# Performance work log

Hardware: AMD Instinct MI355X
Metric: run time of the kernel (lower is better)

## Reference

```python
import jax, jax.numpy as jnp
import numpy as np

BN_EPS = 1e-5
NN_CHUNK = 1024  # unknown points processed per distance-matrix tile


def _batch_ids(cnt, total):
    # contiguous per-batch layout -> batch id of each point via cumsum/searchsorted
    return jnp.searchsorted(jnp.cumsum(cnt), jnp.arange(total), side='right')


def three_nn(unknown, known, ub_id, kb_id):
    """Ragged brute-force 3-NN. Returns (squared dists [N,3], global idx [N,3])."""
    N = unknown.shape[0]
    nchunk = N // NN_CHUNK
    u = unknown.reshape(nchunk, NN_CHUNK, 3)
    ub = ub_id.reshape(nchunk, NN_CHUNK)

    def body(args):
        uc, bc = args
        d2 = jnp.sum((uc[:, None, :] - known[None, :, :]) ** 2, axis=-1)  # [chunk, M]
        d2 = jnp.where(bc[:, None] == kb_id[None, :], d2, jnp.inf)  # mask cross-batch pairs
        neg_d, idx = jax.lax.top_k(-d2, 3)
        return -neg_d, idx

    d2, idx = jax.lax.map(body, (u, ub))
    return d2.reshape(N, 3), idx.reshape(N, 3)


def three_interpolate(known_feats, idx, weight):
    # gather [N,3,C] then inverse-distance weighted sum -> [N,C]
    gathered = known_feats[idx]  # [N,3,C]
    return jnp.einsum('nkc,nk->nc', gathered, weight)


def conv_bn_relu(x, W, gamma, beta):
    # 1x1 Conv2d over [1,C,N,1] == pointwise matmul; BN (training stats) over points
    h = x @ W.T  # [N, C_out]
    mean = jnp.mean(h, axis=0)
    var = jnp.mean((h - mean) ** 2, axis=0)  # biased, as torch BN normalization
    h = (h - mean) * jax.lax.rsqrt(var + BN_EPS) * gamma + beta
    return jax.nn.relu(h)


def setup_inputs() -> dict:
    key = jax.random.key(0)
    ks = jax.random.split(key, 10)
    B, Nper, Mper, C1, C2 = 4, 16384, 4096, 128, 256
    N, M = B * Nper, B * Mper
    unknown = jax.random.normal(ks[0], (N, 3), jnp.float32) * 10.0
    known = jax.random.normal(ks[1], (M, 3), jnp.float32) * 10.0
    unknown_feats = jax.random.normal(ks[2], (N, C1), jnp.float32)
    known_feats = jax.random.normal(ks[3], (M, C2), jnp.float32)
    unknown_batch_cnt = jnp.full((B,), Nper, jnp.int32)
    known_batch_cnt = jnp.full((B,), Mper, jnp.int32)
    Cin = C1 + C2  # 384
    W1 = jax.random.normal(ks[4], (256, Cin), jnp.float32) * (1.0 / np.sqrt(Cin))
    W2 = jax.random.normal(ks[5], (256, 256), jnp.float32) * (1.0 / np.sqrt(256))
    g1 = jnp.ones((256,), jnp.float32); b1 = jnp.zeros((256,), jnp.float32)
    g2 = jnp.ones((256,), jnp.float32); b2 = jnp.zeros((256,), jnp.float32)
    return {"unknown": unknown, "unknown_batch_cnt": unknown_batch_cnt,
            "known": known, "known_batch_cnt": known_batch_cnt,
            "unknown_feats": unknown_feats, "known_feats": known_feats,
            "W1": W1, "g1": g1, "b1": b1, "W2": W2, "g2": g2, "b2": b2}


def reference(unknown, unknown_batch_cnt, known, known_batch_cnt,
              unknown_feats, known_feats, W1, g1, b1, W2, g2, b2):
    ub_id = _batch_ids(unknown_batch_cnt, unknown.shape[0])
    kb_id = _batch_ids(known_batch_cnt, known.shape[0])
    dist, idx = three_nn(unknown, known, ub_id, kb_id)  # squared dists, as CUDA kernel
    dist_recip = 1.0 / (dist + 1e-8)
    weight = dist_recip / jnp.sum(dist_recip, axis=-1, keepdims=True)
    interpolated = three_interpolate(known_feats, idx, weight)  # [N, C2]
    new_features = jnp.concatenate([interpolated, unknown_feats], axis=1)  # [N, C2+C1]
    new_features = conv_bn_relu(new_features, W1, g1, b1)
    new_features = conv_bn_relu(new_features, W2, g2, b2)
    return new_features  # [N, 256]
```

## Files before the change

### kernel.cpp

```cpp
#include <hip/hip_runtime.h>
#include <math.h>

typedef __attribute__((ext_vector_type(8))) short short8;
typedef __attribute__((ext_vector_type(4))) float f32x4;

#define INF 3.0e38f

__device__ __forceinline__ unsigned short f2bf(float x) {
    union { float f; unsigned u; } v; v.f = x;
    unsigned r = v.u + 0x7FFF + ((v.u >> 16) & 1);
    return (unsigned short)(r >> 16);
}

__device__ __forceinline__ float dist2(float ux, float uy, float uz, float4 k) {
    float dx = ux - k.x, dy = uy - k.y, dz = uz - k.z;
    return __builtin_fmaf(dx, dx, __builtin_fmaf(dy, dy, dz * dz));
}

__global__ __launch_bounds__(256) void knn3_kernel(
    const float* __restrict__ unk, const float* __restrict__ kn,
    const int* __restrict__ ucnt, const int* __restrict__ kcnt,
    int B, int N, float* __restrict__ wgt, int* __restrict__ idxo)
{
    __shared__ float4 kxyz[1024];
    __shared__ float md[4][64][3];
    __shared__ float d2g[64];
    __shared__ unsigned long long mk[4][64][3];

    int tid = threadIdx.x;
    int s = tid >> 6;
    int lane = tid & 63;
    int pbase = blockIdx.x * 64;
    int p = pbase + lane;

    int cum = 0, bb = 0;
    for (int i = 0; i < B; i++) { int c = ucnt[i]; if (pbase >= cum) bb = i; cum += c; }
    int kstart = 0;
    for (int i = 0; i < bb; i++) kstart += kcnt[i];
    int kend = kstart + kcnt[bb];

    float ux = unk[p * 3 + 0], uy = unk[p * 3 + 1], uz = unk[p * 3 + 2];

    float d0 = INF, d1 = INF, d2 = INF;
    auto upd = [&](float e) {
        float m0 = fmaxf(e, d0);
        float m1 = fmaxf(e, d1);
        d0 = fminf(e, d0);
        d1 = fminf(m0, d1);
        d2 = fminf(m1, d2);
    };

    for (int t0g = kstart; t0g < kend; t0g += 1024) {
        int cnt = min(1024, kend - t0g);
        __syncthreads();
        for (int f = tid; f < cnt * 3; f += 256) {
            int pt = f / 3, c = f - pt * 3;
            ((float*)&kxyz[pt])[c] = kn[(size_t)(t0g + pt) * 3 + c];
        }
        __syncthreads();

        int qlen = cnt >> 2;
        int base = s * qlen;
        for (int i = 0; i < qlen; i += 4) {
            float e0 = dist2(ux, uy, uz, kxyz[base + i]);
            float e1 = dist2(ux, uy, uz, kxyz[base + i + 1]);
            float e2 = dist2(ux, uy, uz, kxyz[base + i + 2]);
            float e3 = dist2(ux, uy, uz, kxyz[base + i + 3]);
            upd(e0); upd(e1); upd(e2); upd(e3);
        }
    }

    md[s][lane][0] = d0; md[s][lane][1] = d1; md[s][lane][2] = d2;
    __syncthreads();
    if (tid < 64) {
        float v0 = INF, v1 = INF, v2 = INF;
#pragma unroll
        for (int w = 0; w < 4; w++)
#pragma unroll
            for (int k = 0; k < 3; k++) {
                float e = md[w][tid][k];
                float m0 = fmaxf(e, v0);
                float m1 = fmaxf(e, v1);
                v0 = fminf(e, v0);
                v1 = fminf(m0, v1);
                v2 = fminf(m1, v2);
            }
        d2g[tid] = v2;
    }
    __syncthreads();
    float thr = d2g[lane];

    unsigned long long s0 = ~0ULL, s1 = ~0ULL, s2 = ~0ULL;
    auto insK = [&](unsigned long long k) {
        bool c0 = k < s0;
        unsigned long long t0 = c0 ? k : s0;
        unsigned long long t1 = c0 ? s0 : k;
        bool c1 = t1 < s1;
        unsigned long long u0 = c1 ? t1 : s1;
        unsigned long long u1 = c1 ? s1 : t1;
        s0 = t0; s1 = u0;
        s2 = u1 < s2 ? u1 : s2;
    };
    auto mkkey = [](float e, int gj) {
        return ((unsigned long long)__float_as_uint(e) << 32) | (unsigned)gj;
    };

    for (int t0g = kstart; t0g < kend; t0g += 1024) {
        int cnt = min(1024, kend - t0g);
        __syncthreads();
        for (int f = tid; f < cnt * 3; f += 256) {
            int pt = f / 3, c = f - pt * 3;
            ((float*)&kxyz[pt])[c] = kn[(size_t)(t0g + pt) * 3 + c];
        }
        __syncthreads();

        int qlen = cnt >> 2;
        int base = s * qlen;
        for (int i = 0; i < qlen; i += 4) {
            float e0 = dist2(ux, uy, uz, kxyz[base + i]);
            float e1 = dist2(ux, uy, uz, kxyz[base + i + 1]);
            float e2 = dist2(ux, uy, uz, kxyz[base + i + 2]);
            float e3 = dist2(ux, uy, uz, kxyz[base + i + 3]);
            float m4 = fminf(fminf(e0, e1), fminf(e2, e3));
            if (m4 <= thr) {
                int gj = t0g + base + i;
                insK(mkkey(e0, gj + 0));
                insK(mkkey(e1, gj + 1));
                insK(mkkey(e2, gj + 2));
                insK(mkkey(e3, gj + 3));
            }
        }
    }

    mk[s][lane][0] = s0; mk[s][lane][1] = s1; mk[s][lane][2] = s2;
    __syncthreads();

    if (tid < 64) {
        s0 = s1 = s2 = ~0ULL;
#pragma unroll
        for (int qq = 0; qq < 4; qq++)
#pragma unroll
            for (int kk = 0; kk < 3; kk++)
                insK(mk[qq][tid][kk]);

        float dd0 = __uint_as_float((unsigned)(s0 >> 32));
        float dd1 = __uint_as_float((unsigned)(s1 >> 32));
        float dd2 = __uint_as_float((unsigned)(s2 >> 32));
        float r0 = 1.0f / (dd0 + 1e-8f);
        float r1 = 1.0f / (dd1 + 1e-8f);
        float r2 = 1.0f / (dd2 + 1e-8f);
        float rs = 1.0f / (r0 + r1 + r2);
        int pp = pbase + tid;
        wgt[pp * 3 + 0] = r0 * rs;
        wgt[pp * 3 + 1] = r1 * rs;
        wgt[pp * 3 + 2] = r2 * rs;
        idxo[pp * 3 + 0] = (int)(unsigned)s0;
        idxo[pp * 3 + 1] = (int)(unsigned)s1;
        idxo[pp * 3 + 2] = (int)(unsigned)s2;
    }
}

__global__ __launch_bounds__(256) void build_a1_kernel(
    const float* __restrict__ wgt, const int* __restrict__ idxv,
    const float* __restrict__ kfeat, const float* __restrict__ ufeat,
    unsigned short* __restrict__ A1, int N)
{
    int t = blockIdx.x * 256 + threadIdx.x;
    int p = t >> 6, c4 = t & 63;
    if (p >= N) return;
    float w0 = wgt[p * 3 + 0], w1 = wgt[p * 3 + 1], w2 = wgt[p * 3 + 2];
    int j0 = idxv[p * 3 + 0], j1 = idxv[p * 3 + 1], j2 = idxv[p * 3 + 2];
    float4 v0 = ((const float4*)(kfeat + (size_t)j0 * 256))[c4];
    float4 v1 = ((const float4*)(kfeat + (size_t)j1 * 256))[c4];
    float4 v2 = ((const float4*)(kfeat + (size_t)j2 * 256))[c4];
    ushort4 ob;
    ob.x = f2bf(v0.x * w0 + v1.x * w1 + v2.x * w2);
    ob.y = f2bf(v0.y * w0 + v1.y * w1 + v2.y * w2);
    ob.z = f2bf(v0.z * w0 + v1.z * w1 + v2.z * w2);
    ob.w = f2bf(v0.w * w0 + v1.w * w1 + v2.w * w2);
    *(ushort4*)(A1 + (size_t)p * 384 + c4 * 4) = ob;
    float2 u = ((const float2*)(ufeat + (size_t)p * 128))[c4];
    ushort2 ub; ub.x = f2bf(u.x); ub.y = f2bf(u.y);
    *(ushort2*)(A1 + (size_t)p * 384 + 256 + c4 * 2) = ub;
}

__global__ __launch_bounds__(256) void wconv_kernel(
    const float* __restrict__ W1, const float* __restrict__ W2,
    unsigned short* __restrict__ W1b, unsigned short* __restrict__ W2b,
    int n1, int n2)
{
    int i = blockIdx.x * 256 + threadIdx.x;
    if (i < n1) W1b[i] = f2bf(W1[i]);
    int j = i - n1;
    if (j >= 0 && j < n2) W2b[j] = f2bf(W2[j]);
}

template <int K, int MODE>
__global__ __launch_bounds__(256) void gemm_bf16_kernel(
    const void* __restrict__ Av, const unsigned short* __restrict__ W,
    const float* __restrict__ scale, const float* __restrict__ shift,
    float* __restrict__ C, float* __restrict__ gsum, float* __restrict__ gsq)
{
    __shared__ unsigned short As[128 * 40];
    __shared__ unsigned short Bs[128 * 40];
    __shared__ float colsum[128];
    __shared__ float colsq[128];

    int tid = threadIdx.x;
    int w = tid >> 6, lane = tid & 63;
    int r = w >> 1, cq = w & 1;
    int m16 = lane & 15, q = lane >> 4;
    int bm = blockIdx.x * 128, bn = blockIdx.y * 128;

    f32x4 acc[4][4];
#pragma unroll
    for (int i = 0; i < 4; i++)
#pragma unroll
        for (int j = 0; j < 4; j++) acc[i][j] = (f32x4){0.f, 0.f, 0.f, 0.f};

#pragma unroll
    for (int k0 = 0; k0 < K; k0 += 32) {
        __syncthreads();
#pragma unroll
        for (int i = 0; i < 2; i++) {
            int id = tid + i * 256;
            int row = id >> 2, kc = (id & 3) * 8;
            if (MODE == 0) {
                *(short8*)&As[row * 40 + kc] =
                    *(const short8*)((const unsigned short*)Av +
                                     (size_t)(bm + row) * K + k0 + kc);
            } else {
                const float* Af = (const float*)Av;
                float4 v0 = *(const float4*)(Af + (size_t)(bm + row) * K + k0 + kc);
                float4 v1 = *(const float4*)(Af + (size_t)(bm + row) * K + k0 + kc + 4);
                float4 s0 = *(const float4*)(scale + k0 + kc);
                float4 s1 = *(const float4*)(scale + k0 + kc + 4);
                float4 t0 = *(const float4*)(shift + k0 + kc);
                float4 t1 = *(const float4*)(shift + k0 + kc + 4);
                ushort4 o0, o1;
                o0.x = f2bf(fmaxf(v0.x * s0.x + t0.x, 0.f));
                o0.y = f2bf(fmaxf(v0.y * s0.y + t0.y, 0.f));
                o0.z = f2bf(fmaxf(v0.z * s0.z + t0.z, 0.f));
                o0.w = f2bf(fmaxf(v0.w * s0.w + t0.w, 0.f));
                o1.x = f2bf(fmaxf(v1.x * s1.x + t1.x, 0.f));
                o1.y = f2bf(fmaxf(v1.y * s1.y + t1.y, 0.f));
                o1.z = f2bf(fmaxf(v1.z * s1.z + t1.z, 0.f));
                o1.w = f2bf(fmaxf(v1.w * s1.w + t1.w, 0.f));
                *(ushort4*)&As[row * 40 + kc] = o0;
                *(ushort4*)&As[row * 40 + kc + 4] = o1;
            }
            *(short8*)&Bs[row * 40 + kc] =
                *(const short8*)(W + (size_t)(bn + row) * K + k0 + kc);
        }
        __syncthreads();

        short8 af[4], bf[4];
#pragma unroll
        for (int sub = 0; sub < 4; sub++) {
            af[sub] = *(const short8*)&As[(r * 64 + sub * 16 + m16) * 40 + q * 8];
            bf[sub] = *(const short8*)&Bs[(cq * 64 + sub * 16 + m16) * 40 + q * 8];
        }
#pragma unroll
        for (int sm = 0; sm < 4; sm++)
#pragma unroll
            for (int sn = 0; sn < 4; sn++)
                acc[sm][sn] = __builtin_amdgcn_mfma_f32_16x16x32_bf16(
                    af[sm], bf[sn], acc[sm][sn], 0, 0, 0);
    }

    int row0 = bm + r * 64 + q * 4;
    int col0 = bn + cq * 64 + m16;
#pragma unroll
    for (int sm = 0; sm < 4; sm++)
#pragma unroll
        for (int sn = 0; sn < 4; sn++) {
            f32x4 v = acc[sm][sn];
#pragma unroll
            for (int reg = 0; reg < 4; reg++)
                C[(size_t)(row0 + sm * 16 + reg) * 256 + col0 + sn * 16] = v[reg];
        }

    __syncthreads();
    if (tid < 128) { colsum[tid] = 0.f; colsq[tid] = 0.f; }
    __syncthreads();
#pragma unroll
    for (int sn = 0; sn < 4; sn++) {
        float sacc = 0.f, qacc = 0.f;
#pragma unroll
        for (int sm = 0; sm < 4; sm++) {
            f32x4 v = acc[sm][sn];
#pragma unroll
            for (int reg = 0; reg < 4; reg++) {
                sacc += v[reg];
                qacc += v[reg] * v[reg];
            }
        }
        int lc = cq * 64 + sn * 16 + m16;
        atomicAdd(&colsum[lc], sacc);
        atomicAdd(&colsq[lc], qacc);
    }
    __syncthreads();
    if (tid < 128) {
        atomicAdd(&gsum[bn + tid], colsum[tid]);
        atomicAdd(&gsq[bn + tid], colsq[tid]);
    }
}

__global__ void bn_finalize_kernel(
    const float* __restrict__ sum, const float* __restrict__ sumsq,
    const float* __restrict__ g, const float* __restrict__ bta, float invN,
    float* __restrict__ scale, float* __restrict__ shift)
{
    int c = threadIdx.x;
    float mean = sum[c] * invN;
    float var = sumsq[c] * invN - mean * mean;
    float sc = g[c] * rsqrtf(var + 1e-5f);
    scale[c] = sc;
    shift[c] = bta[c] - mean * sc;
}

__global__ __launch_bounds__(256) void final_act_kernel(
    const float* __restrict__ h2, const float* __restrict__ scale,
    const float* __restrict__ shift, float* __restrict__ out, int total4)
{
    int i = blockIdx.x * 256 + threadIdx.x;
    if (i >= total4) return;
    int c4 = i & 63;
    float4 v = ((const float4*)h2)[i];
    float4 s = ((const float4*)scale)[c4];
    float4 t = ((const float4*)shift)[c4];
    float4 o;
    o.x = fmaxf(v.x * s.x + t.x, 0.0f);
    o.y = fmaxf(v.y * s.y + t.y, 0.0f);
    o.z = fmaxf(v.z * s.z + t.z, 0.0f);
    o.w = fmaxf(v.w * s.w + t.w, 0.0f);
    ((float4*)out)[i] = o;
}

extern "C" void kernel_launch(void* const* d_in, const int* in_sizes, int n_in,
                              void* d_out, int out_size, void* d_ws, size_t ws_size,
                              hipStream_t stream)
{
    const float* unknown = (const float*)d_in[0];
    const int*   ucnt    = (const int*)d_in[1];
    const float* known   = (const float*)d_in[2];
    const int*   kcnt    = (const int*)d_in[3];
    const float* ufeat   = (const float*)d_in[4];
    const float* kfeat   = (const float*)d_in[5];
    const float* W1      = (const float*)d_in[6];
    const float* g1      = (const float*)d_in[7];
    const float* b1      = (const float*)d_in[8];
    const float* W2      = (const float*)d_in[9];
    const float* g2      = (const float*)d_in[10];
    const float* b2      = (const float*)d_in[11];

    int N = in_sizes[0] / 3;
    int B = in_sizes[1];

    char* ws = (char*)d_ws;
    size_t off = 0;
    float* wgt = (float*)(ws + off);            off += (size_t)N * 3 * 4;
    int*   idxb = (int*)(ws + off);             off += (size_t)N * 3 * 4;
    float* stats = (float*)(ws + off);          off += 8 * 256 * 4;
    float* sum1 = stats,         *sq1 = stats + 256;
    float* scale1 = stats + 512, *shift1 = stats + 768;
    float* sum2 = stats + 1024,  *sq2 = stats + 1280;
    float* scale2 = stats + 1536, *shift2 = stats + 1792;
    unsigned short* W1b = (unsigned short*)(ws + off);  off += 256 * 384 * 2;
    unsigned short* W2b = (unsigned short*)(ws + off);  off += 256 * 256 * 2;
    off = (off + 255) & ~(size_t)255;
    unsigned short* A1 = (unsigned short*)(ws + off);
    float* h2 = (float*)(ws + off);
    float* h1 = (float*)d_out;

    hipMemsetAsync(stats, 0, 8 * 256 * 4, stream);

    knn3_kernel<<<N / 64, 256, 0, stream>>>(unknown, known, ucnt, kcnt,
                                            B, N, wgt, idxb);
    wconv_kernel<<<(256 * 384 + 256 * 256 + 255) / 256, 256, 0, stream>>>(
        W1, W2, W1b, W2b, 256 * 384, 256 * 256);
    build_a1_kernel<<<N / 4, 256, 0, stream>>>(wgt, idxb, kfeat, ufeat, A1, N);
    gemm_bf16_kernel<384, 0><<<dim3(N / 128, 2), 256, 0, stream>>>(
        A1, W1b, nullptr, nullptr, h1, sum1, sq1);
    bn_finalize_kernel<<<1, 256, 0, stream>>>(sum1, sq1, g1, b1, 1.0f / N,
                                              scale1, shift1);
    gemm_bf16_kernel<256, 1><<<dim3(N / 128, 2), 256, 0, stream>>>(
        h1, W2b, scale1, shift1, h2, sum2, sq2);
    bn_finalize_kernel<<<1, 256, 0, stream>>>(sum2, sq2, g2, b2, 1.0f / N,
                                              scale2, shift2);
    final_act_kernel<<<N / 4, 256, 0, stream>>>(h2, scale2, shift2,
                                                (float*)d_out, N * 64);
}
```

Before: 413.6 us.

## Read known points via wave-uniform scalar loads instead of LDS staging in kNN

```diff
diff --git a/kernel.cpp b/kernel.cpp
--- a/kernel.cpp
+++ b/kernel.cpp
@@ -12,23 +12,17 @@
     return (unsigned short)(r >> 16);
 }
 
-__device__ __forceinline__ float dist2(float ux, float uy, float uz, float4 k) {
-    float dx = ux - k.x, dy = uy - k.y, dz = uz - k.z;
-    return __builtin_fmaf(dx, dx, __builtin_fmaf(dy, dy, dz * dz));
-}
-
 __global__ __launch_bounds__(256) void knn3_kernel(
     const float* __restrict__ unk, const float* __restrict__ kn,
     const int* __restrict__ ucnt, const int* __restrict__ kcnt,
     int B, int N, float* __restrict__ wgt, int* __restrict__ idxo)
 {
-    __shared__ float4 kxyz[1024];
     __shared__ float md[4][64][3];
     __shared__ float d2g[64];
     __shared__ unsigned long long mk[4][64][3];
 
     int tid = threadIdx.x;
-    int s = tid >> 6;
+    int s = __builtin_amdgcn_readfirstlane(tid >> 6);
     int lane = tid & 63;
     int pbase = blockIdx.x * 64;
     int p = pbase + lane;
@@ -40,6 +34,10 @@
     int kend = kstart + kcnt[bb];
 
     float ux = unk[p * 3 + 0], uy = unk[p * 3 + 1], uz = unk[p * 3 + 2];
+
+    int qlen = (kend - kstart) >> 2;
+    int jbase = kstart + s * qlen;
+    const float* kq = kn + (size_t)jbase * 3;
 
     float d0 = INF, d1 = INF, d2 = INF;
     auto upd = [&](float e) {
@@ -50,24 +48,18 @@
         d2 = fminf(m1, d2);
     };
 
-    for (int t0g = kstart; t0g < kend; t0g += 1024) {
-        int cnt = min(1024, kend - t0g);
-        __syncthreads();
-        for (int f = tid; f < cnt * 3; f += 256) {
-            int pt = f / 3, c = f - pt * 3;
-            ((float*)&kxyz[pt])[c] = kn[(size_t)(t0g + pt) * 3 + c];
-        }
-        __syncthreads();
-
-        int qlen = cnt >> 2;
-        int base = s * qlen;
-        for (int i = 0; i < qlen; i += 4) {
-            float e0 = dist2(ux, uy, uz, kxyz[base + i]);
-            float e1 = dist2(ux, uy, uz, kxyz[base + i + 1]);
-            float e2 = dist2(ux, uy, uz, kxyz[base + i + 2]);
-            float e3 = dist2(ux, uy, uz, kxyz[base + i + 3]);
-            upd(e0); upd(e1); upd(e2); upd(e3);
-        }
+    for (int i = 0; i < qlen; i += 8) {
+        float e[8];
+#pragma unroll
+        for (int c = 0; c < 8; c++) {
+            float kx = kq[(i + c) * 3 + 0];
+            float ky = kq[(i + c) * 3 + 1];
+            float kz = kq[(i + c) * 3 + 2];
+            float dx = kx - ux, dy = ky - uy, dz = kz - uz;
+            e[c] = __builtin_fmaf(dx, dx, __builtin_fmaf(dy, dy, dz * dz));
+        }
+#pragma unroll
+        for (int c = 0; c < 8; c++) upd(e[c]);
     }
 
     md[s][lane][0] = d0; md[s][lane][1] = d1; md[s][lane][2] = d2;
@@ -105,30 +97,23 @@
         return ((unsigned long long)__float_as_uint(e) << 32) | (unsigned)gj;
     };
 
-    for (int t0g = kstart; t0g < kend; t0g += 1024) {
-        int cnt = min(1024, kend - t0g);
-        __syncthreads();
-        for (int f = tid; f < cnt * 3; f += 256) {
-            int pt = f / 3, c = f - pt * 3;
-            ((float*)&kxyz[pt])[c] = kn[(size_t)(t0g + pt) * 3 + c];
-        }
-        __syncthreads();
-
-        int qlen = cnt >> 2;
-        int base = s * qlen;
-        for (int i = 0; i < qlen; i += 4) {
-            float e0 = dist2(ux, uy, uz, kxyz[base + i]);
-            float e1 = dist2(ux, uy, uz, kxyz[base + i + 1]);
-            float e2 = dist2(ux, uy, uz, kxyz[base + i + 2]);
-            float e3 = dist2(ux, uy, uz, kxyz[base + i + 3]);
-            float m4 = fminf(fminf(e0, e1), fminf(e2, e3));
-            if (m4 <= thr) {
-                int gj = t0g + base + i;
-                insK(mkkey(e0, gj + 0));
-                insK(mkkey(e1, gj + 1));
-                insK(mkkey(e2, gj + 2));
-                insK(mkkey(e3, gj + 3));
-            }
+    for (int i = 0; i < qlen; i += 4) {
+        float e[4];
+#pragma unroll
+        for (int c = 0; c < 4; c++) {
+            float kx = kq[(i + c) * 3 + 0];
+            float ky = kq[(i + c) * 3 + 1];
+            float kz = kq[(i + c) * 3 + 2];
+            float dx = kx - ux, dy = ky - uy, dz = kz - uz;
+            e[c] = __builtin_fmaf(dx, dx, __builtin_fmaf(dy, dy, dz * dz));
+        }
+        float m4 = fminf(fminf(e[0], e[1]), fminf(e[2], e[3]));
+        if (m4 <= thr) {
+            int gj = jbase + i;
+            insK(mkkey(e[0], gj + 0));
+            insK(mkkey(e[1], gj + 1));
+            insK(mkkey(e[2], gj + 2));
+            insK(mkkey(e[3], gj + 3));
         }
     }
 
```

Measured after the change: 395.5 us. 4.4% less time.
